# Optimization experiments

Measured on AMD Instinct MI355X. Metric: run time of the kernel, lower is better.

## Reference

```python
import jax, jax.numpy as jnp
import numpy as np

N = 50000
E = 800000
F_IN = 128
HEADS = 8
HID = 16
CLASSES = 40
NEG_SLOPE = 0.2


def setup_inputs() -> dict:
    key = jax.random.key(0)
    ks = jax.random.split(key, 10)
    return {
        "x": jax.random.normal(ks[0], (N, F_IN), jnp.float32),
        "edge_index": jax.random.randint(ks[1], (2, E), 0, N, jnp.int64),
        "W1": jax.random.normal(ks[2], (F_IN, HEADS * HID), jnp.float32) * 0.1,
        "a_src1": jax.random.normal(ks[3], (HEADS, HID), jnp.float32) * 0.1,
        "a_dst1": jax.random.normal(ks[4], (HEADS, HID), jnp.float32) * 0.1,
        "b1": jax.random.normal(ks[5], (HEADS * HID,), jnp.float32) * 0.1,
        "W2": jax.random.normal(ks[6], (HEADS * HID, CLASSES), jnp.float32) * 0.1,
        "a_src2": jax.random.normal(ks[7], (1, CLASSES), jnp.float32) * 0.1,
        "a_dst2": jax.random.normal(ks[8], (1, CLASSES), jnp.float32) * 0.1,
        "b2": jax.random.normal(ks[9], (CLASSES,), jnp.float32) * 0.1,
    }


def gat_conv(x, src, dst, W, a_src, a_dst, bias, heads, out_ch, concat):
    # x: [N, in] -> h: [N, H, C]
    h = (x @ W).reshape(N, heads, out_ch)
    e_src = jnp.einsum("nhc,hc->nh", h, a_src)  # [N, H]
    e_dst = jnp.einsum("nhc,hc->nh", h, a_dst)
    alpha = e_src[src] + e_dst[dst]             # [E, H]
    alpha = jax.nn.leaky_relu(alpha, NEG_SLOPE)
    # segment softmax over incoming edges of each dst node
    amax = jax.ops.segment_max(alpha, dst, num_segments=N)
    alpha = jnp.exp(alpha - amax[dst])
    denom = jax.ops.segment_sum(alpha, dst, num_segments=N)
    alpha = alpha / (denom[dst] + 1e-16)
    msg = h[src] * alpha[:, :, None]            # [E, H, C]
    out = jax.ops.segment_sum(msg, dst, num_segments=N)  # [N, H, C]
    out = out.reshape(N, heads * out_ch) if concat else out.mean(axis=1)
    return out + bias


def reference(x, edge_index, W1, a_src1, a_dst1, b1, W2, a_src2, a_dst2, b2):
    # PyG GATConv adds self-loops by default
    loops = jnp.arange(N, dtype=edge_index.dtype)
    src = jnp.concatenate([edge_index[0], loops])
    dst = jnp.concatenate([edge_index[1], loops])
    # inference: dropout layers are identity
    h = gat_conv(x, src, dst, W1, a_src1, a_dst1, b1, HEADS, HID, concat=True)
    h = jax.nn.elu(h)
    out = gat_conv(h, src, dst, W2, a_src2, a_dst2, b2, 1, CLASSES, concat=False)
    return out
```

## Files before the change

### kernel.cpp

```cpp
#include <hip/hip_runtime.h>
#include <math.h>

#define NN 50000
#define EE 800000
#define ET (EE + NN)
#define F_IN 128
#define HEADS 8
#define HID 16
#define C1 (HEADS * HID)
#define CLASSES 40
#define NEG_SLOPE 0.2f
#define LOG2E 1.4426950408889634f

#define NCHUNKS ((NN + 1023) / 1024)
#define NHIST 64
#define EPB (EE / NHIST)
#define LHN 25088

typedef __attribute__((ext_vector_type(8))) short bf16x8;
typedef __attribute__((ext_vector_type(4))) float f32x4;
typedef __attribute__((ext_vector_type(8))) _Float16 h16x8;
typedef __attribute__((ext_vector_type(2))) _Float16 h16x2;

__device__ __forceinline__ unsigned cvtpk(float a, float b) {
    unsigned r;
    asm("v_cvt_pk_bf16_f32 %0, %1, %2" : "=v"(r) : "v"(a), "v"(b));
    return r;
}
__device__ __forceinline__ float fexp2(float x) {
    float r;
    asm("v_exp_f32 %0, %1\n\ts_nop 0" : "=v"(r) : "v"(x));
    return r;
}
__device__ __forceinline__ float bflo(unsigned u) { return __uint_as_float(u << 16); }
__device__ __forceinline__ float bfhi(unsigned u) { return __uint_as_float(u & 0xffff0000u); }
__device__ __forceinline__ float lrelu(float a) { return fmaxf(a, NEG_SLOPE * a); }
__device__ __forceinline__ unsigned short bf1(float a) { return (unsigned short)cvtpk(a, a); }
__device__ __forceinline__ float bf1f(float a) { return bflo(cvtpk(a, a)); }
__device__ __forceinline__ bf16x8 pack8(float f0, float f1, float f2, float f3,
                                        float f4, float f5, float f6, float f7) {
    union { unsigned u[4]; bf16x8 v; } U;
    U.u[0] = cvtpk(f0, f1);
    U.u[1] = cvtpk(f2, f3);
    U.u[2] = cvtpk(f4, f5);
    U.u[3] = cvtpk(f6, f7);
    return U.v;
}

__global__ void prep_kernel(const float* __restrict__ W1,
                            const float* __restrict__ as1, const float* __restrict__ ad1,
                            const float* __restrict__ W2,
                            const float* __restrict__ as2, const float* __restrict__ ad2,
                            const int* __restrict__ ei,
                            unsigned short* __restrict__ va1h, unsigned short* __restrict__ va1l,
                            unsigned short* __restrict__ va2b,
                            unsigned short* __restrict__ W1b, unsigned short* __restrict__ W2b,
                            unsigned* __restrict__ partial) {
    const int tid = threadIdx.x;
    const int b = blockIdx.x;
    if (b >= 3) {
        __shared__ unsigned lhist[LHN];
        for (int i = tid; i < LHN; i += 256) lhist[i] = 0;
        __syncthreads();
        const int hb = b - 3;
        const int* dp = ei + EE + hb * EPB;
        for (int e0 = tid * 4; e0 < EPB; e0 += 1024) {
            int4 d4 = *(const int4*)(dp + e0);
            atomicAdd(&lhist[(unsigned)d4.x >> 1], 1u << ((d4.x & 1) << 4));
            atomicAdd(&lhist[(unsigned)d4.y >> 1], 1u << ((d4.y & 1) << 4));
            atomicAdd(&lhist[(unsigned)d4.z >> 1], 1u << ((d4.z & 1) << 4));
            atomicAdd(&lhist[(unsigned)d4.w >> 1], 1u << ((d4.w & 1) << 4));
        }
        __syncthreads();
        unsigned* pb = partial + (size_t)hb * LHN;
        for (int i = tid; i < LHN; i += 256) pb[i] = lhist[i];
        return;
    }
    if (b == 1) {
        for (int f = tid; f < 2048; f += 256) {
            const int lane = f & 63, kc = (f >> 6) & 3, ntw = f >> 8;
            const int q = lane >> 4, c = lane & 15;
            const int col = ntw * 16 + c;
            const int k0 = kc * 32 + q * 8;
            const float* wp = W1 + (size_t)k0 * C1 + col;
            *(bf16x8*)(W1b + (size_t)f * 8) =
                pack8(wp[0], wp[C1], wp[2 * C1], wp[3 * C1],
                      wp[4 * C1], wp[5 * C1], wp[6 * C1], wp[7 * C1]);
        }
        return;
    }
    if (b == 2) {
        for (int f = tid; f < 768; f += 256) {
            const int lane = f & 63, kc = (f >> 6) & 3, nt = f >> 8;
            const int q = lane >> 4, c = lane & 15;
            const int col = nt * 16 + c;
            const int k0 = kc * 32 + q * 8;
            bf16x8 v = 0;
            if (col < CLASSES) {
                const float* wp = W2 + (size_t)k0 * CLASSES + col;
                v = pack8(wp[0], wp[CLASSES], wp[2 * CLASSES], wp[3 * CLASSES],
                          wp[4 * CLASSES], wp[5 * CLASSES], wp[6 * CLASSES], wp[7 * CLASSES]);
            }
            *(bf16x8*)(W2b + (size_t)f * 8) = v;
        }
        return;
    }
    {
        const int k = tid >> 1, half = tid & 1;
        const float* wrow = W1 + (size_t)k * C1 + half * 64;
        #pragma unroll
        for (int hh = 0; hh < 4; ++hh) {
            const int h = half * 4 + hh;
            float s = 0.f, d = 0.f;
            #pragma unroll
            for (int t = 0; t < 16; ++t) {
                float wv = wrow[hh * 16 + t];
                s += wv * as1[h * HID + t];
                d += wv * ad1[h * HID + t];
            }
            s *= LOG2E; d *= LOG2E;
            va1h[h * 128 + k]       = bf1(s);
            va1l[h * 128 + k]       = bf1(s - bf1f(s));
            va1h[(h + 8) * 128 + k] = bf1(d);
            va1l[(h + 8) * 128 + k] = bf1(d - bf1f(d));
        }
    }
    if (tid < C1) {
        const float* wrow = W2 + (size_t)tid * CLASSES;
        float s = 0.f, d = 0.f;
        #pragma unroll
        for (int c2 = 0; c2 < CLASSES; ++c2) {
            float wv = wrow[c2];
            s += wv * as2[c2];
            d += wv * ad2[c2];
        }
        s *= LOG2E; d *= LOG2E;
        va2b[0 * 128 + tid] = bf1(s);
        va2b[1 * 128 + tid] = bf1(s - bf1f(s));
        va2b[2 * 128 + tid] = bf1(d);
        va2b[3 * 128 + tid] = bf1(d - bf1f(d));
    }
}

__global__ __launch_bounds__(256, 4)
void gemm1_kernel(const float* __restrict__ x,
                  const unsigned short* __restrict__ W1b,
                  const unsigned short* __restrict__ va1h,
                  const unsigned short* __restrict__ va1l,
                  _Float16* __restrict__ h1h,
                  float* __restrict__ e_src, float* __restrict__ e_dst) {
    const int tid = threadIdx.x;
    const int w = tid >> 6, lane = tid & 63;
    const int q = lane >> 4, c = lane & 15;
    const int m0 = (blockIdx.x * 4 + w) * 16;

    int row = m0 + c;
    if (row > NN - 1) row = NN - 1;
    bf16x8 afrag[4];
    #pragma unroll
    for (int kc = 0; kc < 4; ++kc) {
        const float* xp = x + (size_t)row * F_IN + kc * 32 + q * 8;
        float4 p0 = *(const float4*)xp;
        float4 p1 = *(const float4*)(xp + 4);
        afrag[kc] = pack8(p0.x, p0.y, p0.z, p0.w, p1.x, p1.y, p1.z, p1.w);
    }

    {
        f32x4 acce = {0.f, 0.f, 0.f, 0.f};
        #pragma unroll
        for (int kc = 0; kc < 4; ++kc) {
            const int coloff = kc * 32 + q * 8;
            bf16x8 beh = *(const bf16x8*)(va1h + c * 128 + coloff);
            bf16x8 bel = *(const bf16x8*)(va1l + c * 128 + coloff);
            acce = __builtin_amdgcn_mfma_f32_16x16x32_bf16(afrag[kc], beh, acce, 0, 0, 0);
            acce = __builtin_amdgcn_mfma_f32_16x16x32_bf16(afrag[kc], bel, acce, 0, 0, 0);
        }
        float* ep = (c < 8) ? e_src : e_dst;
        const int cc = c & 7;
        #pragma unroll
        for (int r = 0; r < 4; ++r) {
            const int ro = m0 + q * 4 + r;
            if (ro < NN) ep[(size_t)ro * HEADS + cc] = acce[r];
        }
    }

    #pragma unroll 2
    for (int nt = 0; nt < 8; ++nt) {
        bf16x8 bf0 = *(const bf16x8*)(W1b + (size_t)((nt * 4 + 0) * 64 + lane) * 8);
        bf16x8 bf1_ = *(const bf16x8*)(W1b + (size_t)((nt * 4 + 1) * 64 + lane) * 8);
        bf16x8 bf2 = *(const bf16x8*)(W1b + (size_t)((nt * 4 + 2) * 64 + lane) * 8);
        bf16x8 bf3 = *(const bf16x8*)(W1b + (size_t)((nt * 4 + 3) * 64 + lane) * 8);
        f32x4 a = {0.f, 0.f, 0.f, 0.f};
        a = __builtin_amdgcn_mfma_f32_16x16x32_bf16(afrag[0], bf0, a, 0, 0, 0);
        a = __builtin_amdgcn_mfma_f32_16x16x32_bf16(afrag[1], bf1_, a, 0, 0, 0);
        a = __builtin_amdgcn_mfma_f32_16x16x32_bf16(afrag[2], bf2, a, 0, 0, 0);
        a = __builtin_amdgcn_mfma_f32_16x16x32_bf16(afrag[3], bf3, a, 0, 0, 0);
        #pragma unroll
        for (int r = 0; r < 4; ++r) {
            const int ro = m0 + q * 4 + r;
            if (ro < NN) h1h[(size_t)ro * C1 + nt * 16 + c] = (_Float16)a[r];
        }
    }
}

__global__ void scan1_kernel(const unsigned* __restrict__ partial, int* __restrict__ deg,
                             int* __restrict__ rowptr, int* __restrict__ bsum) {
    __shared__ int sh[256];
    const int tid = threadIdx.x;
    const int base = blockIdx.x * 1024 + tid * 4;
    const unsigned short* pu = (const unsigned short*)partial;
    int t0 = 0, t1 = 0, t2 = 0, t3 = 0;
    #pragma unroll 8
    for (int b = 0; b < NHIST; ++b) {
        ushort4 p = *(const ushort4*)(pu + (size_t)b * (LHN * 2) + base);
        t0 += p.x; t1 += p.y; t2 += p.z; t3 += p.w;
    }
    int v[4], s[4];
    v[0] = (base + 0 < NN) ? t0 + 1 : 0;
    v[1] = (base + 1 < NN) ? t1 + 1 : 0;
    v[2] = (base + 2 < NN) ? t2 + 1 : 0;
    v[3] = (base + 3 < NN) ? t3 + 1 : 0;
    #pragma unroll
    for (int j = 0; j < 4; ++j)
        if (base + j < NN) deg[base + j] = v[j];
    s[0] = v[0]; s[1] = s[0] + v[1]; s[2] = s[1] + v[2]; s[3] = s[2] + v[3];
    int T = s[3];
    sh[tid] = T;
    __syncthreads();
    for (int off = 1; off < 256; off <<= 1) {
        int xv = (tid >= off) ? sh[tid - off] : 0;
        __syncthreads();
        sh[tid] += xv;
        __syncthreads();
    }
    int excl = sh[tid] - T;
    #pragma unroll
    for (int j = 0; j < 4; ++j)
        if (base + j < NN) rowptr[base + j] = excl + s[j] - v[j];
    if (tid == 255) bsum[blockIdx.x] = sh[255];
}

__global__ void scan3_kernel(int* __restrict__ rowptr, const int* __restrict__ bsum,
                             int* __restrict__ cursor, unsigned short* __restrict__ csr) {
    __shared__ int ex[64];
    const int tid = threadIdx.x;
    if (tid < 64) {
        int v = (tid < NCHUNKS) ? bsum[tid] : 0;
        int s = v;
        #pragma unroll
        for (int off = 1; off < 64; off <<= 1) {
            int xv = __shfl_up(s, off);
            if (tid >= off) s += xv;
        }
        ex[tid] = s - v;
    }
    __syncthreads();
    int i = blockIdx.x * blockDim.x + tid;
    if (i >= NN) return;
    int rp = rowptr[i] + ex[i >> 10];
    rowptr[i] = rp;
    cursor[i] = rp + 1;
    csr[rp] = (unsigned short)i;
}

__global__ void fill_kernel(const int* __restrict__ ei, int* __restrict__ cursor,
                            unsigned short* __restrict__ csr) {
    int base = (blockIdx.x * blockDim.x + threadIdx.x) * 4;
    if (base >= EE) return;
    int4 s4 = *(const int4*)(ei + base);
    int4 d4 = *(const int4*)(ei + EE + base);
    int p0 = atomicAdd(&cursor[d4.x], 1);
    int p1 = atomicAdd(&cursor[d4.y], 1);
    int p2 = atomicAdd(&cursor[d4.z], 1);
    int p3 = atomicAdd(&cursor[d4.w], 1);
    csr[p0] = (unsigned short)s4.x;
    csr[p1] = (unsigned short)s4.y;
    csr[p2] = (unsigned short)s4.z;
    csr[p3] = (unsigned short)s4.w;
}

__global__ void agg1_kernel(const _Float16* __restrict__ h1h,
                            const float* __restrict__ e_src, const float* __restrict__ e_dst,
                            const int* __restrict__ rowptr, const int* __restrict__ deg,
                            const unsigned short* __restrict__ csr,
                            const float* __restrict__ b1, unsigned short* __restrict__ hmid) {
    const int tid = threadIdx.x;
    const int lane = tid & 63;
    const int l = lane & 15;
    const int d = blockIdx.x * 16 + (tid >> 4);
    const int hd = l >> 1;
    const float ed = e_dst[(size_t)d * HEADS + hd];
    const int start = rowptr[d];
    const int cnt = deg[d];

    float denom = 0.f;
    float acc[8] = {0.f, 0.f, 0.f, 0.f, 0.f, 0.f, 0.f, 0.f};

    for (int i = 0; i < cnt; i += 4) {
        const bool v1 = i + 1 < cnt, v2 = i + 2 < cnt, v3 = i + 3 < cnt;
        int s0 = csr[start + i];
        int s1 = csr[start + (v1 ? i + 1 : i)];
        int s2 = csr[start + (v2 ? i + 2 : i)];
        int s3 = csr[start + (v3 ? i + 3 : i)];
        float es0 = e_src[(size_t)s0 * HEADS + hd];
        float es1 = e_src[(size_t)s1 * HEADS + hd];
        float es2 = e_src[(size_t)s2 * HEADS + hd];
        float es3 = e_src[(size_t)s3 * HEADS + hd];
        h16x8 g0 = *(const h16x8*)(h1h + (size_t)s0 * C1 + 8 * l);
        h16x8 g1 = *(const h16x8*)(h1h + (size_t)s1 * C1 + 8 * l);
        h16x8 g2 = *(const h16x8*)(h1h + (size_t)s2 * C1 + 8 * l);
        h16x8 g3 = *(const h16x8*)(h1h + (size_t)s3 * C1 + 8 * l);
        float w0 = fexp2(lrelu(es0 + ed));
        float w1 = v1 ? fexp2(lrelu(es1 + ed)) : 0.f;
        float w2 = v2 ? fexp2(lrelu(es2 + ed)) : 0.f;
        float w3 = v3 ? fexp2(lrelu(es3 + ed)) : 0.f;
        denom += (w0 + w1) + (w2 + w3);
        #pragma unroll
        for (int j = 0; j < 8; ++j) {
            acc[j] = fmaf((float)g0[j], w0, acc[j]);
            acc[j] = fmaf((float)g1[j], w1, acc[j]);
            acc[j] = fmaf((float)g2[j], w2, acc[j]);
            acc[j] = fmaf((float)g3[j], w3, acc[j]);
        }
    }
    const float inv = 1.f / (denom + 1e-16f);
    float o[8];
    #pragma unroll
    for (int k = 0; k < 8; ++k) {
        float t = acc[k] * inv + b1[8 * l + k];
        o[k] = (t > 0.f) ? t : fexp2(t * LOG2E) - 1.f;
    }
    uint4 st;
    st.x = cvtpk(o[0], o[1]);
    st.y = cvtpk(o[2], o[3]);
    st.z = cvtpk(o[4], o[5]);
    st.w = cvtpk(o[6], o[7]);
    *(uint4*)(hmid + (size_t)d * C1 + 8 * l) = st;
}

__global__ __launch_bounds__(256, 4)
void gemm2_kernel(const unsigned short* __restrict__ hmid,
                  const unsigned short* __restrict__ W2b,
                  const unsigned short* __restrict__ va2b,
                  _Float16* __restrict__ h2h,
                  float* __restrict__ e_src, float* __restrict__ e_dst) {
    const int tid = threadIdx.x;
    const int w = tid >> 6, lane = tid & 63;
    const int q = lane >> 4, c = lane & 15;

    const int m0 = (blockIdx.x * 4 + w) * 16;
    if (m0 >= NN) return;
    int row = m0 + c;
    if (row > NN - 1) row = NN - 1;
    bf16x8 afrag[4];
    #pragma unroll
    for (int kc = 0; kc < 4; ++kc)
        afrag[kc] = *(const bf16x8*)(hmid + (size_t)row * C1 + kc * 32 + q * 8);

    bf16x8 bfrag[3][4];
    #pragma unroll
    for (int nt = 0; nt < 3; ++nt)
        #pragma unroll
        for (int kc = 0; kc < 4; ++kc)
            bfrag[nt][kc] = *(const bf16x8*)(W2b + (size_t)((nt * 4 + kc) * 64 + lane) * 8);
    bf16x8 bfe[4];
    #pragma unroll
    for (int kc = 0; kc < 4; ++kc) {
        bf16x8 bb = 0;
        if (c < 4) bb = *(const bf16x8*)(va2b + c * 128 + kc * 32 + q * 8);
        bfe[kc] = bb;
    }

    f32x4 acc[3] = {{0.f,0.f,0.f,0.f},{0.f,0.f,0.f,0.f},{0.f,0.f,0.f,0.f}};
    f32x4 acce = {0.f, 0.f, 0.f, 0.f};
    #pragma unroll
    for (int kc = 0; kc < 4; ++kc) {
        acc[0] = __builtin_amdgcn_mfma_f32_16x16x32_bf16(afrag[kc], bfrag[0][kc], acc[0], 0, 0, 0);
        acc[1] = __builtin_amdgcn_mfma_f32_16x16x32_bf16(afrag[kc], bfrag[1][kc], acc[1], 0, 0, 0);
        acc[2] = __builtin_amdgcn_mfma_f32_16x16x32_bf16(afrag[kc], bfrag[2][kc], acc[2], 0, 0, 0);
        acce   = __builtin_amdgcn_mfma_f32_16x16x32_bf16(afrag[kc], bfe[kc],      acce,   0, 0, 0);
    }
    #pragma unroll
    for (int r = 0; r < 4; ++r) {
        const int ro = m0 + q * 4 + r;
        float v = acce[r] + __shfl_xor(acce[r], 1);
        if (ro < NN) {
            #pragma unroll
            for (int nt = 0; nt < 3; ++nt) {
                const int col = nt * 16 + c;
                if (col < CLASSES)
                    h2h[(size_t)ro * CLASSES + col] = (_Float16)acc[nt][r];
            }
            if (c == 0) e_src[ro] = v;
            if (c == 2) e_dst[ro] = v;
        }
    }
}

__global__ void agg2_kernel(const _Float16* __restrict__ h2h,
                            const float* __restrict__ e_src, const float* __restrict__ e_dst,
                            const int* __restrict__ rowptr, const int* __restrict__ deg,
                            const unsigned short* __restrict__ csr,
                            const float* __restrict__ b2, float* __restrict__ out) {
    const int tid = threadIdx.x;
    const int wv = tid >> 6, lane = tid & 63;
    const int eg = lane / 20;
    const int c  = lane % 20;
    const int d = blockIdx.x * 12 + wv * 3 + eg;
    const bool live = (eg < 3) && (d < NN);
    const int dcl = live ? d : 0;
    const float ed = e_dst[dcl];
    const int start = rowptr[dcl];
    const int cnt = live ? deg[dcl] : 0;

    float denom = 0.f, acc0 = 0.f, acc1 = 0.f;
    for (int i = 0; i < cnt; i += 4) {
        const bool v1 = i + 1 < cnt, v2 = i + 2 < cnt, v3 = i + 3 < cnt;
        int s0 = csr[start + i];
        int s1 = csr[start + (v1 ? i + 1 : i)];
        int s2 = csr[start + (v2 ? i + 2 : i)];
        int s3 = csr[start + (v3 ? i + 3 : i)];
        float es0 = e_src[s0], es1 = e_src[s1], es2 = e_src[s2], es3 = e_src[s3];
        h16x2 g0 = *(const h16x2*)(h2h + (size_t)s0 * CLASSES + 2 * c);
        h16x2 g1 = *(const h16x2*)(h2h + (size_t)s1 * CLASSES + 2 * c);
        h16x2 g2 = *(const h16x2*)(h2h + (size_t)s2 * CLASSES + 2 * c);
        h16x2 g3 = *(const h16x2*)(h2h + (size_t)s3 * CLASSES + 2 * c);
        float w0 = fexp2(lrelu(es0 + ed));
        float w1 = v1 ? fexp2(lrelu(es1 + ed)) : 0.f;
        float w2 = v2 ? fexp2(lrelu(es2 + ed)) : 0.f;
        float w3 = v3 ? fexp2(lrelu(es3 + ed)) : 0.f;
        denom += (w0 + w1) + (w2 + w3);
        acc0 = fmaf((float)g0[0], w0, acc0); acc1 = fmaf((float)g0[1], w0, acc1);
        acc0 = fmaf((float)g1[0], w1, acc0); acc1 = fmaf((float)g1[1], w1, acc1);
        acc0 = fmaf((float)g2[0], w2, acc0); acc1 = fmaf((float)g2[1], w2, acc1);
        acc0 = fmaf((float)g3[0], w3, acc0); acc1 = fmaf((float)g3[1], w3, acc1);
    }
    if (live) {
        const float inv = 1.f / (denom + 1e-16f);
        float2 o;
        o.x = acc0 * inv + b2[2 * c];
        o.y = acc1 * inv + b2[2 * c + 1];
        *(float2*)(out + (size_t)d * CLASSES + 2 * c) = o;
    }
}

extern "C" void kernel_launch(void* const* d_in, const int* in_sizes, int n_in,
                              void* d_out, int out_size, void* d_ws, size_t ws_size,
                              hipStream_t stream) {
    const float* x      = (const float*)d_in[0];
    const int*   ei     = (const int*)d_in[1];
    const float* W1     = (const float*)d_in[2];
    const float* a_src1 = (const float*)d_in[3];
    const float* a_dst1 = (const float*)d_in[4];
    const float* b1     = (const float*)d_in[5];
    const float* W2     = (const float*)d_in[6];
    const float* a_src2 = (const float*)d_in[7];
    const float* a_dst2 = (const float*)d_in[8];
    const float* b2     = (const float*)d_in[9];
    float* out = (float*)d_out;

    char* ws = (char*)d_ws;
    size_t off = 0;
    auto alloc = [&](size_t bytes) { char* p = ws + off; off += (bytes + 255) & ~(size_t)255; return p; };
    _Float16* h1h = (_Float16*)alloc((size_t)NN * C1 * 2);
    _Float16* h2h = (_Float16*)alloc((size_t)NN * CLASSES * 2);
    unsigned short* hmidb = (unsigned short*)alloc((size_t)NN * C1 * 2);
    float* e_src1 = (float*)alloc((size_t)NN * HEADS * 4);
    float* e_dst1 = (float*)alloc((size_t)NN * HEADS * 4);
    float* e_src2 = (float*)alloc((size_t)NN * 4);
    float* e_dst2 = (float*)alloc((size_t)NN * 4);
    int*   deg    = (int*)alloc((size_t)NN * 4);
    int*   rowptr = (int*)alloc((size_t)NN * 4);
    int*   cursor = (int*)alloc((size_t)NN * 4);
    unsigned short* csr  = (unsigned short*)alloc((size_t)ET * 2);
    int*   bsum   = (int*)alloc(256 * 4);
    unsigned short* va1h = (unsigned short*)alloc(16 * 128 * 2);
    unsigned short* va1l = (unsigned short*)alloc(16 * 128 * 2);
    unsigned short* va2b = (unsigned short*)alloc(4 * 128 * 2);
    unsigned short* W1b  = (unsigned short*)alloc(2048 * 8 * 2);
    unsigned short* W2b  = (unsigned short*)alloc(768 * 8 * 2);
    unsigned* partial    = (unsigned*)alloc((size_t)NHIST * LHN * 4);

    prep_kernel<<<3 + NHIST, 256, 0, stream>>>(W1, a_src1, a_dst1, W2, a_src2, a_dst2, ei,
                                               va1h, va1l, va2b, W1b, W2b, partial);
    gemm1_kernel<<<(NN + 63) / 64, 256, 0, stream>>>(x, W1b, va1h, va1l,
                                                     h1h, e_src1, e_dst1);
    scan1_kernel<<<NCHUNKS, 256, 0, stream>>>(partial, deg, rowptr, bsum);
    scan3_kernel<<<(NN + 255) / 256, 256, 0, stream>>>(rowptr, bsum, cursor, csr);
    fill_kernel<<<(EE / 4 + 255) / 256, 256, 0, stream>>>(ei, cursor, csr);

    agg1_kernel<<<NN / 16, 256, 0, stream>>>(h1h, e_src1, e_dst1, rowptr, deg, csr, b1, hmidb);

    gemm2_kernel<<<(NN + 63) / 64, 256, 0, stream>>>(hmidb, W2b, va2b, h2h, e_src2, e_dst2);
    agg2_kernel<<<(NN + 11) / 12, 256, 0, stream>>>(h2h, e_src2, e_dst2, rowptr, deg, csr, b2, out);
}
```

Measured before the change: 241.3 us.

## Fuse GEMM1 with CSR fill and deepen gather unroll in aggregation kernels

Merges the first-layer GEMM and the CSR fill pass into one launch, with even blocks doing GEMM and odd blocks doing edge scatter, so the compute-bound and atomic-bound work overlap on the device. The scan kernels now run before the GEMM. Both aggregation kernels go to 64-thread blocks and unroll the neighbor loop to 8 edges per iteration, putting more gathers in flight per wave to hide memory latency. In exchange, register pressure rises and the tiny blocks add scheduling overhead.

```diff
diff --git a/kernel.cpp b/kernel.cpp
--- a/kernel.cpp
+++ b/kernel.cpp
@@ -16,6 +16,7 @@
 #define NHIST 64
 #define EPB (EE / NHIST)
 #define LHN 25088
+#define GB ((NN + 63) / 64)
 
 typedef __attribute__((ext_vector_type(8))) short bf16x8;
 typedef __attribute__((ext_vector_type(4))) float f32x4;
@@ -142,17 +143,97 @@
     }
 }
 
+__global__ void scan1_kernel(const unsigned* __restrict__ partial, int* __restrict__ deg,
+                             int* __restrict__ rowptr, int* __restrict__ bsum) {
+    __shared__ int sh[256];
+    const int tid = threadIdx.x;
+    const int base = blockIdx.x * 1024 + tid * 4;
+    const unsigned short* pu = (const unsigned short*)partial;
+    int t0 = 0, t1 = 0, t2 = 0, t3 = 0;
+    #pragma unroll 8
+    for (int b = 0; b < NHIST; ++b) {
+        ushort4 p = *(const ushort4*)(pu + (size_t)b * (LHN * 2) + base);
+        t0 += p.x; t1 += p.y; t2 += p.z; t3 += p.w;
+    }
+    int v[4], s[4];
+    v[0] = (base + 0 < NN) ? t0 + 1 : 0;
+    v[1] = (base + 1 < NN) ? t1 + 1 : 0;
+    v[2] = (base + 2 < NN) ? t2 + 1 : 0;
+    v[3] = (base + 3 < NN) ? t3 + 1 : 0;
+    #pragma unroll
+    for (int j = 0; j < 4; ++j)
+        if (base + j < NN) deg[base + j] = v[j];
+    s[0] = v[0]; s[1] = s[0] + v[1]; s[2] = s[1] + v[2]; s[3] = s[2] + v[3];
+    int T = s[3];
+    sh[tid] = T;
+    __syncthreads();
+    for (int off = 1; off < 256; off <<= 1) {
+        int xv = (tid >= off) ? sh[tid - off] : 0;
+        __syncthreads();
+        sh[tid] += xv;
+        __syncthreads();
+    }
+    int excl = sh[tid] - T;
+    #pragma unroll
+    for (int j = 0; j < 4; ++j)
+        if (base + j < NN) rowptr[base + j] = excl + s[j] - v[j];
+    if (tid == 255) bsum[blockIdx.x] = sh[255];
+}
+
+__global__ void scan3_kernel(int* __restrict__ rowptr, const int* __restrict__ bsum,
+                             int* __restrict__ cursor, unsigned short* __restrict__ csr) {
+    __shared__ int ex[64];
+    const int tid = threadIdx.x;
+    if (tid < 64) {
+        int v = (tid < NCHUNKS) ? bsum[tid] : 0;
+        int s = v;
+        #pragma unroll
+        for (int off = 1; off < 64; off <<= 1) {
+            int xv = __shfl_up(s, off);
+            if (tid >= off) s += xv;
+        }
+        ex[tid] = s - v;
+    }
+    __syncthreads();
+    int i = blockIdx.x * blockDim.x + tid;
+    if (i >= NN) return;
+    int rp = rowptr[i] + ex[i >> 10];
+    rowptr[i] = rp;
+    cursor[i] = rp + 1;
+    csr[rp] = (unsigned short)i;
+}
+
 __global__ __launch_bounds__(256, 4)
-void gemm1_kernel(const float* __restrict__ x,
-                  const unsigned short* __restrict__ W1b,
-                  const unsigned short* __restrict__ va1h,
-                  const unsigned short* __restrict__ va1l,
-                  _Float16* __restrict__ h1h,
-                  float* __restrict__ e_src, float* __restrict__ e_dst) {
-    const int tid = threadIdx.x;
+void gemm1_fill_kernel(const float* __restrict__ x,
+                       const unsigned short* __restrict__ W1b,
+                       const unsigned short* __restrict__ va1h,
+                       const unsigned short* __restrict__ va1l,
+                       const int* __restrict__ ei,
+                       int* __restrict__ cursor, unsigned short* __restrict__ csr,
+                       _Float16* __restrict__ h1h,
+                       float* __restrict__ e_src, float* __restrict__ e_dst) {
+    const int bid = blockIdx.x;
+    const int tid = threadIdx.x;
+    if (bid & 1) {
+        int base = ((bid >> 1) * 256 + tid) * 4;
+        if (base < EE) {
+            int4 s4 = *(const int4*)(ei + base);
+            int4 d4 = *(const int4*)(ei + EE + base);
+            int p0 = atomicAdd(&cursor[d4.x], 1);
+            int p1 = atomicAdd(&cursor[d4.y], 1);
+            int p2 = atomicAdd(&cursor[d4.z], 1);
+            int p3 = atomicAdd(&cursor[d4.w], 1);
+            csr[p0] = (unsigned short)s4.x;
+            csr[p1] = (unsigned short)s4.y;
+            csr[p2] = (unsigned short)s4.z;
+            csr[p3] = (unsigned short)s4.w;
+        }
+        return;
+    }
+    const int gemmb = bid >> 1;
     const int w = tid >> 6, lane = tid & 63;
     const int q = lane >> 4, c = lane & 15;
-    const int m0 = (blockIdx.x * 4 + w) * 16;
+    const int m0 = (gemmb * 4 + w) * 16;
 
     int row = m0 + c;
     if (row > NN - 1) row = NN - 1;
@@ -203,91 +284,15 @@
     }
 }
 
-__global__ void scan1_kernel(const unsigned* __restrict__ partial, int* __restrict__ deg,
-                             int* __restrict__ rowptr, int* __restrict__ bsum) {
-    __shared__ int sh[256];
-    const int tid = threadIdx.x;
-    const int base = blockIdx.x * 1024 + tid * 4;
-    const unsigned short* pu = (const unsigned short*)partial;
-    int t0 = 0, t1 = 0, t2 = 0, t3 = 0;
-    #pragma unroll 8
-    for (int b = 0; b < NHIST; ++b) {
-        ushort4 p = *(const ushort4*)(pu + (size_t)b * (LHN * 2) + base);
-        t0 += p.x; t1 += p.y; t2 += p.z; t3 += p.w;
-    }
-    int v[4], s[4];
-    v[0] = (base + 0 < NN) ? t0 + 1 : 0;
-    v[1] = (base + 1 < NN) ? t1 + 1 : 0;
-    v[2] = (base + 2 < NN) ? t2 + 1 : 0;
-    v[3] = (base + 3 < NN) ? t3 + 1 : 0;
-    #pragma unroll
-    for (int j = 0; j < 4; ++j)
-        if (base + j < NN) deg[base + j] = v[j];
-    s[0] = v[0]; s[1] = s[0] + v[1]; s[2] = s[1] + v[2]; s[3] = s[2] + v[3];
-    int T = s[3];
-    sh[tid] = T;
-    __syncthreads();
-    for (int off = 1; off < 256; off <<= 1) {
-        int xv = (tid >= off) ? sh[tid - off] : 0;
-        __syncthreads();
-        sh[tid] += xv;
-        __syncthreads();
-    }
-    int excl = sh[tid] - T;
-    #pragma unroll
-    for (int j = 0; j < 4; ++j)
-        if (base + j < NN) rowptr[base + j] = excl + s[j] - v[j];
-    if (tid == 255) bsum[blockIdx.x] = sh[255];
-}
-
-__global__ void scan3_kernel(int* __restrict__ rowptr, const int* __restrict__ bsum,
-                             int* __restrict__ cursor, unsigned short* __restrict__ csr) {
-    __shared__ int ex[64];
-    const int tid = threadIdx.x;
-    if (tid < 64) {
-        int v = (tid < NCHUNKS) ? bsum[tid] : 0;
-        int s = v;
-        #pragma unroll
-        for (int off = 1; off < 64; off <<= 1) {
-            int xv = __shfl_up(s, off);
-            if (tid >= off) s += xv;
-        }
-        ex[tid] = s - v;
-    }
-    __syncthreads();
-    int i = blockIdx.x * blockDim.x + tid;
-    if (i >= NN) return;
-    int rp = rowptr[i] + ex[i >> 10];
-    rowptr[i] = rp;
-    cursor[i] = rp + 1;
-    csr[rp] = (unsigned short)i;
-}
-
-__global__ void fill_kernel(const int* __restrict__ ei, int* __restrict__ cursor,
-                            unsigned short* __restrict__ csr) {
-    int base = (blockIdx.x * blockDim.x + threadIdx.x) * 4;
-    if (base >= EE) return;
-    int4 s4 = *(const int4*)(ei + base);
-    int4 d4 = *(const int4*)(ei + EE + base);
-    int p0 = atomicAdd(&cursor[d4.x], 1);
-    int p1 = atomicAdd(&cursor[d4.y], 1);
-    int p2 = atomicAdd(&cursor[d4.z], 1);
-    int p3 = atomicAdd(&cursor[d4.w], 1);
-    csr[p0] = (unsigned short)s4.x;
-    csr[p1] = (unsigned short)s4.y;
-    csr[p2] = (unsigned short)s4.z;
-    csr[p3] = (unsigned short)s4.w;
-}
-
-__global__ void agg1_kernel(const _Float16* __restrict__ h1h,
-                            const float* __restrict__ e_src, const float* __restrict__ e_dst,
-                            const int* __restrict__ rowptr, const int* __restrict__ deg,
-                            const unsigned short* __restrict__ csr,
-                            const float* __restrict__ b1, unsigned short* __restrict__ hmid) {
-    const int tid = threadIdx.x;
-    const int lane = tid & 63;
-    const int l = lane & 15;
-    const int d = blockIdx.x * 16 + (tid >> 4);
+__global__ __launch_bounds__(64)
+void agg1_kernel(const _Float16* __restrict__ h1h,
+                 const float* __restrict__ e_src, const float* __restrict__ e_dst,
+                 const int* __restrict__ rowptr, const int* __restrict__ deg,
+                 const unsigned short* __restrict__ csr,
+                 const float* __restrict__ b1, unsigned short* __restrict__ hmid) {
+    const int tid = threadIdx.x;
+    const int l = tid & 15;
+    const int d = blockIdx.x * 4 + (tid >> 4);
     const int hd = l >> 1;
     const float ed = e_dst[(size_t)d * HEADS + hd];
     const int start = rowptr[d];
@@ -296,31 +301,31 @@
     float denom = 0.f;
     float acc[8] = {0.f, 0.f, 0.f, 0.f, 0.f, 0.f, 0.f, 0.f};
 
-    for (int i = 0; i < cnt; i += 4) {
-        const bool v1 = i + 1 < cnt, v2 = i + 2 < cnt, v3 = i + 3 < cnt;
-        int s0 = csr[start + i];
-        int s1 = csr[start + (v1 ? i + 1 : i)];
-        int s2 = csr[start + (v2 ? i + 2 : i)];
-        int s3 = csr[start + (v3 ? i + 3 : i)];
-        float es0 = e_src[(size_t)s0 * HEADS + hd];
-        float es1 = e_src[(size_t)s1 * HEADS + hd];
-        float es2 = e_src[(size_t)s2 * HEADS + hd];
-        float es3 = e_src[(size_t)s3 * HEADS + hd];
-        h16x8 g0 = *(const h16x8*)(h1h + (size_t)s0 * C1 + 8 * l);
-        h16x8 g1 = *(const h16x8*)(h1h + (size_t)s1 * C1 + 8 * l);
-        h16x8 g2 = *(const h16x8*)(h1h + (size_t)s2 * C1 + 8 * l);
-        h16x8 g3 = *(const h16x8*)(h1h + (size_t)s3 * C1 + 8 * l);
-        float w0 = fexp2(lrelu(es0 + ed));
-        float w1 = v1 ? fexp2(lrelu(es1 + ed)) : 0.f;
-        float w2 = v2 ? fexp2(lrelu(es2 + ed)) : 0.f;
-        float w3 = v3 ? fexp2(lrelu(es3 + ed)) : 0.f;
-        denom += (w0 + w1) + (w2 + w3);
-        #pragma unroll
-        for (int j = 0; j < 8; ++j) {
-            acc[j] = fmaf((float)g0[j], w0, acc[j]);
-            acc[j] = fmaf((float)g1[j], w1, acc[j]);
-            acc[j] = fmaf((float)g2[j], w2, acc[j]);
-            acc[j] = fmaf((float)g3[j], w3, acc[j]);
+    for (int i = 0; i < cnt; i += 8) {
+        int s[8];
+        #pragma unroll
+        for (int e = 0; e < 8; ++e)
+            s[e] = csr[start + ((i + e < cnt) ? i + e : i)];
+        float es[8];
+        #pragma unroll
+        for (int e = 0; e < 8; ++e)
+            es[e] = e_src[(size_t)s[e] * HEADS + hd];
+        h16x8 g[8];
+        #pragma unroll
+        for (int e = 0; e < 8; ++e)
+            g[e] = *(const h16x8*)(h1h + (size_t)s[e] * C1 + 8 * l);
+        float w[8];
+        #pragma unroll
+        for (int e = 0; e < 8; ++e) {
+            float we = fexp2(lrelu(es[e] + ed));
+            w[e] = (i + e < cnt) ? we : 0.f;
+            denom += w[e];
+        }
+        #pragma unroll
+        for (int e = 0; e < 8; ++e) {
+            #pragma unroll
+            for (int j = 0; j < 8; ++j)
+                acc[j] = fmaf((float)g[e][j], w[e], acc[j]);
         }
     }
     const float inv = 1.f / (denom + 1e-16f);
@@ -397,16 +402,16 @@
     }
 }
 
-__global__ void agg2_kernel(const _Float16* __restrict__ h2h,
-                            const float* __restrict__ e_src, const float* __restrict__ e_dst,
-                            const int* __restrict__ rowptr, const int* __restrict__ deg,
-                            const unsigned short* __restrict__ csr,
-                            const float* __restrict__ b2, float* __restrict__ out) {
-    const int tid = threadIdx.x;
-    const int wv = tid >> 6, lane = tid & 63;
-    const int eg = lane / 20;
-    const int c  = lane % 20;
-    const int d = blockIdx.x * 12 + wv * 3 + eg;
+__global__ __launch_bounds__(64)
+void agg2_kernel(const _Float16* __restrict__ h2h,
+                 const float* __restrict__ e_src, const float* __restrict__ e_dst,
+                 const int* __restrict__ rowptr, const int* __restrict__ deg,
+                 const unsigned short* __restrict__ csr,
+                 const float* __restrict__ b2, float* __restrict__ out) {
+    const int tid = threadIdx.x;
+    const int eg = tid / 20;
+    const int c  = tid % 20;
+    const int d = blockIdx.x * 3 + eg;
     const bool live = (eg < 3) && (d < NN);
     const int dcl = live ? d : 0;
     const float ed = e_dst[dcl];
@@ -414,26 +419,31 @@
     const int cnt = live ? deg[dcl] : 0;
 
     float denom = 0.f, acc0 = 0.f, acc1 = 0.f;
-    for (int i = 0; i < cnt; i += 4) {
-        const bool v1 = i + 1 < cnt, v2 = i + 2 < cnt, v3 = i + 3 < cnt;
-        int s0 = csr[start + i];
-        int s1 = csr[start + (v1 ? i + 1 : i)];
-        int s2 = csr[start + (v2 ? i + 2 : i)];
-        int s3 = csr[start + (v3 ? i + 3 : i)];
-        float es0 = e_src[s0], es1 = e_src[s1], es2 = e_src[s2], es3 = e_src[s3];
-        h16x2 g0 = *(const h16x2*)(h2h + (size_t)s0 * CLASSES + 2 * c);
-        h16x2 g1 = *(const h16x2*)(h2h + (size_t)s1 * CLASSES + 2 * c);
-        h16x2 g2 = *(const h16x2*)(h2h + (size_t)s2 * CLASSES + 2 * c);
-        h16x2 g3 = *(const h16x2*)(h2h + (size_t)s3 * CLASSES + 2 * c);
-        float w0 = fexp2(lrelu(es0 + ed));
-        float w1 = v1 ? fexp2(lrelu(es1 + ed)) : 0.f;
-        float w2 = v2 ? fexp2(lrelu(es2 + ed)) : 0.f;
-        float w3 = v3 ? fexp2(lrelu(es3 + ed)) : 0.f;
-        denom += (w0 + w1) + (w2 + w3);
-        acc0 = fmaf((float)g0[0], w0, acc0); acc1 = fmaf((float)g0[1], w0, acc1);
-        acc0 = fmaf((float)g1[0], w1, acc0); acc1 = fmaf((float)g1[1], w1, acc1);
-        acc0 = fmaf((float)g2[0], w2, acc0); acc1 = fmaf((float)g2[1], w2, acc1);
-        acc0 = fmaf((float)g3[0], w3, acc0); acc1 = fmaf((float)g3[1], w3, acc1);
+    for (int i = 0; i < cnt; i += 8) {
+        int s[8];
+        #pragma unroll
+        for (int e = 0; e < 8; ++e)
+            s[e] = csr[start + ((i + e < cnt) ? i + e : i)];
+        float es[8];
+        #pragma unroll
+        for (int e = 0; e < 8; ++e)
+            es[e] = e_src[s[e]];
+        h16x2 g[8];
+        #pragma unroll
+        for (int e = 0; e < 8; ++e)
+            g[e] = *(const h16x2*)(h2h + (size_t)s[e] * CLASSES + 2 * c);
+        float w[8];
+        #pragma unroll
+        for (int e = 0; e < 8; ++e) {
+            float we = fexp2(lrelu(es[e] + ed));
+            w[e] = (i + e < cnt) ? we : 0.f;
+            denom += w[e];
+        }
+        #pragma unroll
+        for (int e = 0; e < 8; ++e) {
+            acc0 = fmaf((float)g[e][0], w[e], acc0);
+            acc1 = fmaf((float)g[e][1], w[e], acc1);
+        }
     }
     if (live) {
         const float inv = 1.f / (denom + 1e-16f);
@@ -483,14 +493,13 @@
 
     prep_kernel<<<3 + NHIST, 256, 0, stream>>>(W1, a_src1, a_dst1, W2, a_src2, a_dst2, ei,
                                                va1h, va1l, va2b, W1b, W2b, partial);
-    gemm1_kernel<<<(NN + 63) / 64, 256, 0, stream>>>(x, W1b, va1h, va1l,
-                                                     h1h, e_src1, e_dst1);
     scan1_kernel<<<NCHUNKS, 256, 0, stream>>>(partial, deg, rowptr, bsum);
     scan3_kernel<<<(NN + 255) / 256, 256, 0, stream>>>(rowptr, bsum, cursor, csr);
-    fill_kernel<<<(EE / 4 + 255) / 256, 256, 0, stream>>>(ei, cursor, csr);
-
-    agg1_kernel<<<NN / 16, 256, 0, stream>>>(h1h, e_src1, e_dst1, rowptr, deg, csr, b1, hmidb);
+    gemm1_fill_kernel<<<2 * GB, 256, 0, stream>>>(x, W1b, va1h, va1l, ei, cursor, csr,
+                                                  h1h, e_src1, e_dst1);
+
+    agg1_kernel<<<NN / 4, 64, 0, stream>>>(h1h, e_src1, e_dst1, rowptr, deg, csr, b1, hmidb);
 
     gemm2_kernel<<<(NN + 63) / 64, 256, 0, stream>>>(hmidb, W2b, va2b, h2h, e_src2, e_dst2);
-    agg2_kernel<<<(NN + 11) / 12, 256, 0, stream>>>(h2h, e_src2, e_dst2, rowptr, deg, csr, b2, out);
-}
+    agg2_kernel<<<(NN + 2) / 3, 64, 0, stream>>>(h2h, e_src2, e_dst2, rowptr, deg, csr, b2, out);
+}
```

Measured after the change: 217.4 us. 9.9% less time.
